# Kernel tuning notes

Hardware: AMD Instinct MI355X
Metric: run time of the kernel (lower is better)

## Reference

```python
import jax, jax.numpy as jnp
import numpy as np

# ---- static config (matches init_kwargs) ----
MO = 4            # multiplicity per output irrep: '4x0e+4x1o+4x2e'
NUM_BASIS = 10
HIDDEN = 64
N_NODES = 50000
N_EDGES = 800000

# ---------- numpy-side precompute of real Wigner-3j tensors ----------
def _sh_np(l, v):
    x, y, z = v[..., 0], v[..., 1], v[..., 2]
    if l == 0:
        return np.ones(v.shape[:-1] + (1,))
    if l == 1:
        return np.sqrt(3.0) * np.stack([x, y, z], -1)
    return np.stack([
        np.sqrt(15.0) * x * z,
        np.sqrt(15.0) * x * y,
        np.sqrt(5.0) / 2.0 * (2 * y * y - x * x - z * z),
        np.sqrt(15.0) * y * z,
        np.sqrt(15.0) / 2.0 * (z * z - x * x),
    ], -1)

def _wigner_D_np(l, R):
    # real Wigner-D consistent with _sh_np basis: sh(R v) = D @ sh(v)
    if l == 0:
        return np.ones((1, 1))
    rng = np.random.default_rng(1234 + l)
    V = rng.normal(size=(2 * l + 1, 3))
    V /= np.linalg.norm(V, axis=1, keepdims=True)
    B = _sh_np(l, V).T
    A = _sh_np(l, V @ R.T).T
    return A @ np.linalg.inv(B)

def _w3j_np(l1, l2, l3):
    rng = np.random.default_rng(42)
    rows = []
    for _ in range(3):
        Q, _ = np.linalg.qr(rng.normal(size=(3, 3)))
        if np.linalg.det(Q) < 0:
            Q = Q.copy(); Q[:, 0] *= -1.0
        K = np.kron(np.kron(_wigner_D_np(l1, Q), _wigner_D_np(l2, Q)), _wigner_D_np(l3, Q))
        rows.append(K - np.eye(K.shape[0]))
    _, _, vt = np.linalg.svd(np.concatenate(rows, 0))
    c = vt[-1]
    c = c * np.sign(c[np.argmax(np.abs(c))])
    C = c.reshape(2 * l1 + 1, 2 * l2 + 1, 2 * l3 + 1)
    return C / np.linalg.norm(C)

_SH_IRREPS = [(0, 1), (1, -1), (2, 1)]   # 1x0e + 1x1o + 1x2e
_OUT_IRREPS = [(0, 1), (1, -1), (2, 1)]  # MO x (0e, 1o, 2e)

def _build_tp(mul1, l1, p1):
    # e3nn FullyConnectedTensorProduct instructions ('uvw', component/element norm)
    ins = []
    for (l2, p2) in _SH_IRREPS:
        for io, (lo, po) in enumerate(_OUT_IRREPS):
            if abs(l1 - l2) <= lo <= l1 + l2 and p1 * p2 == po:
                ins.append({'l2': l2, 'lo': lo, 'io': io})
    fan = {}
    for j in ins:
        fan[j['io']] = fan.get(j['io'], 0) + mul1  # mul1 * mul2(=1)
    for j in ins:
        j['pw'] = float(np.sqrt((2 * j['lo'] + 1) / fan[j['io']]))
        j['C'] = _w3j_np(l1, j['l2'], j['lo'])
    return ins

INS_S = _build_tp(1, 0, 1)
INS_P = _build_tp(3, 1, -1)
INS_D = _build_tp(5, 2, 1)
WNUM_S = len(INS_S) * 1 * MO   # 12
WNUM_P = len(INS_P) * 3 * MO   # 48
WNUM_D = len(INS_D) * 5 * MO   # 80

# ---------- jax forward pieces ----------
def _sh_jnp(u):
    # component-normalized real spherical harmonics, lmax=2, e3nn convention
    x, y, z = u[:, 0], u[:, 1], u[:, 2]
    s3, s15, s5 = np.sqrt(3.0), np.sqrt(15.0), np.sqrt(5.0)
    return jnp.stack([
        jnp.ones_like(x),
        s3 * x, s3 * y, s3 * z,
        s15 * x * z, s15 * x * y,
        s5 / 2.0 * (2 * y * y - x * x - z * z),
        s15 * y * z, s15 / 2.0 * (z * z - x * x),
    ], axis=1)

def _soft_one_hot(x, end, number):
    # e3nn soft_one_hot_linspace, basis='smooth_finite', cutoff=True
    values = jnp.linspace(0.0, end, number + 2)
    step = values[1] - values[0]
    values = values[1:-1]
    diff = (x[:, None] - values) / step
    def sus(t):
        return jnp.where(t > 0, jnp.exp(-1.0 / jnp.where(t > 0, t, 1.0)), 0.0)
    return (1.14136 * np.exp(2.0)) * sus(diff + 1.0) * sus(1.0 - diff)

def _fc(x, W1, W2):
    # e3nn FullyConnectedNet([n_in, hidden, n_out], relu): weight/ sqrt(fan_in),
    # relu normalized to second moment 1 (factor sqrt(2))
    h = np.sqrt(2.0) * jax.nn.relu(x @ (W1 / np.sqrt(x.shape[1])))
    return h @ (W2 / np.sqrt(W1.shape[1]))

def _apply_tp(x1, sh, weights, ins, mul1):
    # x1: (E, mul1, 2l1+1); sh: (E, 9); weights: (E, len(ins)*mul1*MO)
    E = x1.shape[0]
    outs = [jnp.zeros((E, MO, 2 * lo + 1), x1.dtype) for lo in (0, 1, 2)]
    off = 0
    for j in ins:
        W = weights[:, off:off + mul1 * MO].reshape(E, mul1, MO)
        off += mul1 * MO
        l2 = j['l2']
        shj = sh[:, l2 * l2:(l2 + 1) * (l2 + 1)]
        C = jnp.asarray(j['C'], x1.dtype)
        outs[j['lo']] = outs[j['lo']] + j['pw'] * jnp.einsum(
            'eui,ej,ijk,euw->ewk', x1, shj, C, W)
    return jnp.concatenate([o.reshape(E, -1) for o in outs], axis=1)  # (E, 36)

def _forward(f_in, pos, W1_s, W2_s, W1_p, W2_p, W1_d, W2_d, row, col, max_radius, num_nodes):
    edge_vec = pos[row] - pos[col]                      # (E, 3)
    r = jnp.sqrt(jnp.sum(edge_vec * edge_vec, axis=1) + 1e-12)
    u = edge_vec / r[:, None]
    sh = _sh_jnp(u)                                     # (E, 9)
    emb = _soft_one_hot(r, float(max_radius), NUM_BASIS) * (NUM_BASIS ** 0.5)
    ws = _fc(emb, W1_s, W2_s)
    wp = _fc(emb, W1_p, W2_p)
    wd = _fc(emb, W1_d, W2_d)
    fm = f_in.reshape(num_nodes, 9, 9, 2)
    # tp(x0) + tp(x1) with identical weights == tp(x0 + x1) by linearity in input1
    x_s = (fm[:, 0:1, 0:1, 0] + fm[:, 0:1, 0:1, 1]).reshape(num_nodes, 1, 1)[row]
    x_p = (fm[:, 1:4, 1:4, 0] + fm[:, 1:4, 1:4, 1]).reshape(num_nodes, 3, 3)[row]
    x_d = (fm[:, 4:9, 4:9, 0] + fm[:, 4:9, 4:9, 1]).reshape(num_nodes, 5, 5)[row]
    out_s = _apply_tp(x_s, sh, ws, INS_S, 1)
    out_p = _apply_tp(x_p, sh, wp, INS_P, 3)
    out_d = _apply_tp(x_d, sh, wd, INS_D, 5)
    summand = jnp.concatenate([out_s, out_p, out_d], axis=1)   # (E, 108)
    f_out = jax.ops.segment_sum(summand, col, num_segments=num_nodes)
    num_neighbors = row.shape[0] / num_nodes
    return f_out / (num_neighbors ** 0.5)

def setup_inputs() -> dict:
    key = jax.random.key(0)
    ks = jax.random.split(key, 9)
    return {
        'f_in': jax.random.normal(ks[0], (N_NODES, 162), jnp.float32),
        'edge_index': jax.random.randint(ks[1], (2, N_EDGES), 0, N_NODES, dtype=jnp.int32),
        'pos': jax.random.normal(ks[2], (N_NODES, 3), jnp.float32),
        'max_radius': 5,
        'num_nodes': N_NODES,
        'W1_s': jax.random.normal(ks[3], (NUM_BASIS, HIDDEN), jnp.float32),
        'W2_s': jax.random.normal(ks[4], (HIDDEN, WNUM_S), jnp.float32),
        'W1_p': jax.random.normal(ks[5], (NUM_BASIS, HIDDEN), jnp.float32),
        'W2_p': jax.random.normal(ks[6], (HIDDEN, WNUM_P), jnp.float32),
        'W1_d': jax.random.normal(ks[7], (NUM_BASIS, HIDDEN), jnp.float32),
        'W2_d': jax.random.normal(ks[8], (HIDDEN, WNUM_D), jnp.float32),
    }

def reference(f_in, edge_index, pos, max_radius, num_nodes, W1_s, W2_s, W1_p, W2_p, W1_d, W2_d):
    return _forward(f_in, pos, W1_s, W2_s, W1_p, W2_p, W1_d, W2_d,
                    edge_index[0], edge_index[1], max_radius, num_nodes)
```

## Files before the change

### kernel.cpp

```cpp
#include <hip/hip_runtime.h>
#include <math.h>

#define TPB 256

#define R10   0.31622776601683794f
#define R30   0.18257418583505536f
#define R30x2 0.36514837167011072f
#define CCA (0.23904572186687872f)
#define CCB (0.20701966780270623f)
#define CCC (0.11952286093343936f)

#define TROW 144
#define RSTR 56

typedef float f4 __attribute__((ext_vector_type(4)));

__device__ __forceinline__ void atomAddF(float* p, float v) {
    __hip_atomic_fetch_add(p, v, __ATOMIC_RELAXED, __HIP_MEMORY_SCOPE_AGENT);
}

__global__ __launch_bounds__(256) void build_rec_count(const float* __restrict__ f_in,
                                                       const float* __restrict__ pos,
                                                       const int* __restrict__ eidx,
                                                       float* __restrict__ rec,
                                                       int* __restrict__ cnt,
                                                       int N, int E) {
    int i = blockIdx.x * 256 + threadIdx.x;
    if (i < N) {
        const float* f = f_in + (size_t)i * 162;
        float* r = rec + (size_t)i * RSTR;
        r[0] = pos[i * 3 + 0]; r[1] = pos[i * 3 + 1]; r[2] = pos[i * 3 + 2];
        float2 v0 = *(const float2*)f;
        r[3] = v0.x + v0.y;
#pragma unroll
        for (int u = 0; u < 3; ++u)
#pragma unroll
            for (int v = 0; v < 3; ++v) {
                float2 a = *(const float2*)(f + ((1 + u) * 9 + (1 + v)) * 2);
                r[4 + u * 3 + v] = a.x + a.y;
            }
#pragma unroll
        for (int u = 0; u < 5; ++u)
#pragma unroll
            for (int v = 0; v < 5; ++v) {
                float2 a = *(const float2*)(f + ((4 + u) * 9 + (4 + v)) * 2);
                r[16 + u * 8 + v] = a.x + a.y;
            }
    }
    if (i < E) atomicAdd(&cnt[eidx[E + i]], 1);
}

__global__ __launch_bounds__(256) void build_table(const float* __restrict__ W1s,
                                                   const float* __restrict__ W2s,
                                                   const float* __restrict__ W1p,
                                                   const float* __restrict__ W2p,
                                                   const float* __restrict__ W1d,
                                                   const float* __restrict__ W2d,
                                                   float* __restrict__ table,
                                                   float Delta, float base) {
    __shared__ float t3[192];
    const int tid = threadIdx.x;
    const float r = (float)blockIdx.x * Delta;

    const float F = (float)(1.14136 * 7.38905609893065 * 3.1622776601683795);
    float qq = r * 2.2f;
    int a0 = (int)floorf(qq) - 1;
    int ac = min(max(a0, 0), 8);
    float d0 = qq - (float)(ac + 1);
    float d0s = d0 * d0;
    float ea = (d0s < 1.f) ? F * expf(-2.f / (1.f - d0s)) : 0.f;
    float d1 = d0 - 1.f;
    float d1s = d1 * d1;
    float eb = (d1s < 1.f) ? F * expf(-2.f / (1.f - d1s)) : 0.f;

    if (tid < 192) {
        int path = tid >> 6, j = tid & 63;
        const float* W1 = (path == 0) ? W1s : (path == 1) ? W1p : W1d;
        float u = W1[ac * 64 + j];
        float v = W1[(ac + 1) * 64 + j];
        t3[tid] = fmaxf(fmaf(eb, v, ea * u), 0.f);
    }
    __syncthreads();
    if (tid >= 140) return;

    const float* W2; const float* t; int M, m; float kf; int newcol;
    if (tid < 12) {
        W2 = W2s; t = t3; M = 12; m = tid; kf = 1.f;
        int kind = m >> 2, w = m & 3;
        newcol = w * 4 + kind;
    } else if (tid < 60) {
        W2 = W2p; t = t3 + 64; M = 48; m = tid - 12;
        kf = (m < 12) ? 0.40824829046386307f
           : (m < 24) ? 0.33333333333333333f
           : (m < 36) ? 1.29099444873580560f
                      : 0.70710678118654752f;
        int kind = m / 12, u = (m % 12) >> 2, w = m & 3;
        newcol = 16 + w * 12 + u * 4 + kind;
    } else {
        W2 = W2d; t = t3 + 128; M = 80; m = tid - 60;
        kf = (m < 20) ? 0.31622776601683794f
           : (m < 40) ? 0.77459666924148340f
           : (m < 60) ? 0.2f
                      : 0.70710678118654752f;
        int kind = m / 20, u = (m % 20) >> 2, w = m & 3;
        newcol = 64 + w * 20 + u * 4 + kind;
    }
    float acc = 0.f;
#pragma unroll 4
    for (int j = 0; j < 64; ++j)
        acc = fmaf(t[j], W2[j * M + m], acc);
    table[(size_t)blockIdx.x * TROW + newcol] = acc * (base * kf);
}

__global__ __launch_bounds__(1024) void scan_kernel(int* data, int N) {
    __shared__ int wsum[16];
    const int tid = threadIdx.x;
    const int lane = tid & 63;
    const int wv = tid >> 6;
    int carry = 0;
    for (int base = 0; base < N; base += 4096) {
        int i0 = base + tid * 4;
        int v0 = (i0 + 0 < N) ? data[i0 + 0] : 0;
        int v1 = (i0 + 1 < N) ? data[i0 + 1] : 0;
        int v2 = (i0 + 2 < N) ? data[i0 + 2] : 0;
        int v3 = (i0 + 3 < N) ? data[i0 + 3] : 0;
        int s = v0 + v1 + v2 + v3;
        int sc = s;
        for (int d = 1; d < 64; d <<= 1) {
            int t = __shfl_up(sc, d);
            if (lane >= d) sc += t;
        }
        if (lane == 63) wsum[wv] = sc;
        __syncthreads();
        int woff = carry, tot = carry;
#pragma unroll
        for (int w = 0; w < 16; ++w) {
            int x = wsum[w];
            if (w < wv) woff += x;
            tot += x;
        }
        int excl = woff + (sc - s);
        if (i0 + 0 < N) data[i0 + 0] = excl;
        excl += v0;
        if (i0 + 1 < N) data[i0 + 1] = excl;
        excl += v1;
        if (i0 + 2 < N) data[i0 + 2] = excl;
        excl += v2;
        if (i0 + 3 < N) data[i0 + 3] = excl;
        carry = tot;
        __syncthreads();
    }
}

__global__ __launch_bounds__(256) void permute_rows(const int* __restrict__ eidx,
                                                    int* __restrict__ cursor,
                                                    int* __restrict__ rows, int E) {
    int e = blockIdx.x * 256 + threadIdx.x;
    if (e < E) {
        int c = eidx[E + e];
        int p = atomicAdd(&cursor[c], 1);
        rows[p] = eidx[e];
    }
}

__global__ __launch_bounds__(256) void gather_kernel(
    const float* __restrict__ rec,
    const int* __restrict__ rows,
    const int* __restrict__ cursor,
    const float* __restrict__ table,
    float* __restrict__ out,
    int N, int NB, float invDelta)
{
    const int bRole = (4 * N + 255) >> 8;
    int bid = blockIdx.x;
    int role = (bid < bRole) ? 2 : (bid < 2 * bRole) ? 1 : 0;
    int lbid = bid - ((role == 2) ? 0 : (role == 1) ? bRole : 2 * bRole);
    int idx = lbid * 256 + threadIdx.x;
    if (idx >= 4 * N) return;
    const int node = idx >> 2;
    const int w = idx & 3;

    const float* rq = rec + (size_t)node * RSTR;
    const float qx = rq[0], qy = rq[1], qz = rq[2];
    const int e0 = (node == 0) ? 0 : cursor[node - 1];
    const int e1 = cursor[node];

    float a0 = 0.f, a1 = 0.f, a2 = 0.f, a3 = 0.f, a4 = 0.f,
          a5 = 0.f, a6 = 0.f, a7 = 0.f, a8 = 0.f;

    for (int p = e0; p < e1; ++p) {
        int row = rows[p];
        const float* rr = rec + (size_t)row * RSTR;
        f4 h0 = *(const f4*)rr;
        float ex = h0[0] - qx, ey = h0[1] - qy, ez = h0[2] - qz;
        float r = sqrtf(ex * ex + ey * ey + ez * ez + 1e-12f);
        float rinv = 1.0f / r;
        float x = ex * rinv, y = ey * rinv, z = ez * rinv;

        float sh1 = 1.7320508075688772f * x;
        float sh2 = 1.7320508075688772f * y;
        float sh3 = 1.7320508075688772f * z;
        float sh4 = 3.8729833462074170f * x * z;
        float sh5 = 3.8729833462074170f * x * y;
        float sh6 = 1.1180339887498949f * (2.f * y * y - x * x - z * z);
        float sh7 = 3.8729833462074170f * y * z;
        float sh8 = 1.9364916731037085f * (z * z - x * x);

        float rn = r * invDelta;
        int bin = (int)floorf(rn);
        float f = rn - (float)bin;
        if (bin >= NB) { bin = NB - 1; f = 1.f; }
        const float* T0 = table + (size_t)bin * TROW;
        const float* T1 = T0 + TROW;

        if (role == 0) {
            f4 ta = *(const f4*)(T0 + w * 4);
            f4 tc = *(const f4*)(T1 + w * 4);
            float ws0 = fmaf(f, tc[0] - ta[0], ta[0]);
            float ws1 = fmaf(f, tc[1] - ta[1], ta[1]);
            float ws2 = fmaf(f, tc[2] - ta[2], ta[2]);
            float X = h0[3];
            a0 = fmaf(X, ws0, a0);
            float t1 = X * ws1;
            a1 = fmaf(t1, sh1, a1);
            a2 = fmaf(t1, sh2, a2);
            a3 = fmaf(t1, sh3, a3);
            float t2 = X * ws2;
            a4 = fmaf(t2, sh4, a4);
            a5 = fmaf(t2, sh5, a5);
            a6 = fmaf(t2, sh6, a6);
            a7 = fmaf(t2, sh7, a7);
            a8 = fmaf(t2, sh8, a8);
        } else if (role == 1) {
            f4 xv0 = *(const f4*)(rr + 4);
            f4 xv1 = *(const f4*)(rr + 8);
            float xp8 = rr[12];
            const float* tp0 = T0 + 16 + w * 12;
            const float* tp1 = T1 + 16 + w * 12;
#pragma unroll
            for (int u = 0; u < 3; ++u) {
                float x0 = (u == 0) ? xv0[0] : (u == 1) ? xv0[3] : xv1[2];
                float x1 = (u == 0) ? xv0[1] : (u == 1) ? xv1[0] : xv1[3];
                float x2 = (u == 0) ? xv0[2] : (u == 1) ? xv1[1] : xp8;
                f4 ta = *(const f4*)(tp0 + u * 4);
                f4 tc = *(const f4*)(tp1 + u * 4);
                f4 wv;
                wv[0] = fmaf(f, tc[0] - ta[0], ta[0]);
                wv[1] = fmaf(f, tc[1] - ta[1], ta[1]);
                wv[2] = fmaf(f, tc[2] - ta[2], ta[2]);
                wv[3] = fmaf(f, tc[3] - ta[3], ta[3]);
                float dot = x0 * sh1 + x1 * sh2 + x2 * sh3;
                float ya0 = R10 * (x0 * sh3 + x2 * sh1);
                float ya1 = R10 * (x0 * sh2 + x1 * sh1);
                float ya2 = R30 * (2.f * x1 * sh2 - x0 * sh1 - x2 * sh3);
                float ya3 = R10 * (x1 * sh3 + x2 * sh2);
                float ya4 = R10 * (x2 * sh3 - x0 * sh1);
                float yb0 = R10 * (x2 * sh4 + x1 * sh5 - x0 * sh8) - R30 * x0 * sh6;
                float yb1 = R10 * (x0 * sh5 + x2 * sh7) + R30x2 * x1 * sh6;
                float yb2 = R10 * (x0 * sh4 + x1 * sh7 + x2 * sh8) - R30 * x2 * sh6;
                a0 = fmaf(dot, wv[1], a0);
                a1 = fmaf(x0, wv[0], fmaf(yb0, wv[3], a1));
                a2 = fmaf(x1, wv[0], fmaf(yb1, wv[3], a2));
                a3 = fmaf(x2, wv[0], fmaf(yb2, wv[3], a3));
                a4 = fmaf(ya0, wv[2], a4);
                a5 = fmaf(ya1, wv[2], a5);
                a6 = fmaf(ya2, wv[2], a6);
                a7 = fmaf(ya3, wv[2], a7);
                a8 = fmaf(ya4, wv[2], a8);
            }
        } else {
            const float* td0 = T0 + 64 + w * 20;
            const float* td1 = T1 + 64 + w * 20;
#pragma unroll
            for (int u = 0; u < 5; ++u) {
                f4 xv = *(const f4*)(rr + 16 + u * 8);
                float x4 = rr[16 + u * 8 + 4];
                float x0 = xv[0], x1 = xv[1], x2 = xv[2], x3 = xv[3];
                f4 ta = *(const f4*)(td0 + u * 4);
                f4 tc = *(const f4*)(td1 + u * 4);
                f4 wv;
                wv[0] = fmaf(f, tc[0] - ta[0], ta[0]);
                wv[1] = fmaf(f, tc[1] - ta[1], ta[1]);
                wv[2] = fmaf(f, tc[2] - ta[2], ta[2]);
                wv[3] = fmaf(f, tc[3] - ta[3], ta[3]);
                float dot = x0 * sh4 + x1 * sh5 + x2 * sh6 + x3 * sh7 + x4 * sh8;
                float yb0 = R10 * (x0 * sh3 + x1 * sh2 - x4 * sh1) - R30 * x2 * sh1;
                float yb1 = R10 * (x1 * sh1 + x3 * sh3) + R30x2 * x2 * sh2;
                float yb2 = R10 * (x0 * sh1 + x3 * sh2 + x4 * sh3) - R30 * x2 * sh3;
                float yc0 = CCA * (x2 * sh4 + x0 * sh6) - CCB * (x1 * sh7 + x3 * sh5);
                float yc1 = CCB * (x1 * sh8 + x4 * sh5 - x0 * sh7 - x3 * sh4)
                          - CCC * (x1 * sh6 + x2 * sh5);
                float yc2 = CCA * (x0 * sh4 - x2 * sh6 + x4 * sh8)
                          - CCC * (x1 * sh5 + x3 * sh7);
                float yc3 = -CCB * (x0 * sh5 + x1 * sh4 + x3 * sh8 + x4 * sh7)
                          - CCC * (x2 * sh7 + x3 * sh6);
                float yc4 = CCB * (x1 * sh5 - x3 * sh7) + CCA * (x2 * sh8 + x4 * sh6);
                a0 = fmaf(dot, wv[2], a0);
                a1 = fmaf(yb0, wv[1], a1);
                a2 = fmaf(yb1, wv[1], a2);
                a3 = fmaf(yb2, wv[1], a3);
                a4 = fmaf(x0, wv[0], fmaf(yc0, wv[3], a4));
                a5 = fmaf(x1, wv[0], fmaf(yc1, wv[3], a5));
                a6 = fmaf(x2, wv[0], fmaf(yc2, wv[3], a6));
                a7 = fmaf(x3, wv[0], fmaf(yc3, wv[3], a7));
                a8 = fmaf(x4, wv[0], fmaf(yc4, wv[3], a8));
            }
        }
    }

    const int obase = (role == 0) ? 0 : (role == 1) ? 36 : 72;
    float* o = out + (size_t)node * 108 + obase;
    o[w] = a0;
    o[4 + w * 3 + 0] = a1;
    o[4 + w * 3 + 1] = a2;
    o[4 + w * 3 + 2] = a3;
    o[16 + w * 5 + 0] = a4;
    o[16 + w * 5 + 1] = a5;
    o[16 + w * 5 + 2] = a6;
    o[16 + w * 5 + 3] = a7;
    o[16 + w * 5 + 4] = a8;
}

template<int M>
__device__ __forceinline__ void fc_eval(const float* sW1T, const float* sW2,
                                        const float emb[12], float* acc)
{
#pragma unroll
    for (int m = 0; m < M; ++m) acc[m] = 0.f;
#pragma unroll 2
    for (int j = 0; j < 64; ++j) {
        const float4* w1r = (const float4*)(sW1T + j * 12);
        float4 A = w1r[0], B = w1r[1], C = w1r[2];
        float t = A.x*emb[0] + A.y*emb[1] + A.z*emb[2] + A.w*emb[3]
                + B.x*emb[4] + B.y*emb[5] + B.z*emb[6] + B.w*emb[7]
                + C.x*emb[8] + C.y*emb[9];
        t = fmaxf(t, 0.f);
        const float4* w2r = (const float4*)(sW2 + j * M);
#pragma unroll
        for (int q = 0; q < M / 4; ++q) {
            float4 V = w2r[q];
            acc[4*q+0] = fmaf(t, V.x, acc[4*q+0]);
            acc[4*q+1] = fmaf(t, V.y, acc[4*q+1]);
            acc[4*q+2] = fmaf(t, V.z, acc[4*q+2]);
            acc[4*q+3] = fmaf(t, V.w, acc[4*q+3]);
        }
    }
}

__global__ __launch_bounds__(TPB) void eqconv_edge_kernel_atomic(
    const float* __restrict__ f_in,
    const int*   __restrict__ eidx,
    const float* __restrict__ pos,
    const float* __restrict__ W1s_g, const float* __restrict__ W2s_g,
    const float* __restrict__ W1p_g, const float* __restrict__ W2p_g,
    const float* __restrict__ W1d_g, const float* __restrict__ W2d_g,
    float* __restrict__ out,
    int E, float snorm)
{
    __shared__ __align__(16) float smem[11264];
    float* tW1s = smem;
    float* tW1p = smem + 768;
    float* tW1d = smem + 1536;
    float* sW2s = smem + 2304;
    float* sW2p = smem + 3072;
    float* sW2d = smem + 6144;

    const int tid = threadIdx.x;
    const float base = 0.05590169943749474f * snorm;

    for (int idx = tid; idx < 768; idx += TPB) {
        int j = idx / 12, i = idx - j * 12;
        tW1s[idx] = (i < 10) ? W1s_g[i * 64 + j] : 0.f;
        tW1p[idx] = (i < 10) ? W1p_g[i * 64 + j] : 0.f;
        tW1d[idx] = (i < 10) ? W1d_g[i * 64 + j] : 0.f;
    }
    for (int idx = tid; idx < 768; idx += TPB)
        sW2s[idx] = W2s_g[idx] * base;
    for (int idx = tid; idx < 3072; idx += TPB) {
        int m = idx % 48;
        float k = (m < 12) ? 0.40824829046386307f
                : (m < 24) ? 0.33333333333333333f
                : (m < 36) ? 1.29099444873580560f
                           : 0.70710678118654752f;
        sW2p[idx] = W2p_g[idx] * (base * k);
    }
    for (int idx = tid; idx < 5120; idx += TPB) {
        int m = idx % 80;
        float k = (m < 20) ? 0.31622776601683794f
                : (m < 40) ? 0.77459666924148340f
                : (m < 60) ? 0.2f
                           : 0.70710678118654752f;
        sW2d[idx] = W2d_g[idx] * (base * k);
    }
    __syncthreads();

    int e = blockIdx.x * TPB + tid;
    if (e >= E) return;

    const int row = eidx[e];
    const int col = eidx[E + e];

    float ex = pos[row * 3 + 0] - pos[col * 3 + 0];
    float ey = pos[row * 3 + 1] - pos[col * 3 + 1];
    float ez = pos[row * 3 + 2] - pos[col * 3 + 2];
    float r = sqrtf(ex * ex + ey * ey + ez * ez + 1e-12f);
    float rinv = 1.0f / r;
    float x = ex * rinv, y = ey * rinv, z = ez * rinv;

    float sh1 = 1.7320508075688772f * x;
    float sh2 = 1.7320508075688772f * y;
    float sh3 = 1.7320508075688772f * z;
    float sh4 = 3.8729833462074170f * x * z;
    float sh5 = 3.8729833462074170f * x * y;
    float sh6 = 1.1180339887498949f * (2.f * y * y - x * x - z * z);
    float sh7 = 3.8729833462074170f * y * z;
    float sh8 = 1.9364916731037085f * (z * z - x * x);

    float emb[12];
    {
        const float F = (float)(1.14136 * 7.38905609893065 * 3.1622776601683795);
        const float inv_step = 2.2f;
#pragma unroll
        for (int i = 0; i < 10; ++i) {
            float v = (float)(i + 1) * (5.0f / 11.0f);
            float d = (r - v) * inv_step;
            float d2 = d * d;
            emb[i] = (d2 < 1.0f) ? F * expf(-2.0f / (1.0f - d2)) : 0.f;
        }
        emb[10] = 0.f; emb[11] = 0.f;
    }

    const float* fr = f_in + (size_t)row * 162;
    float* o = out + (size_t)col * 108;

    {
        float ws[12];
        fc_eval<12>(tW1s, sW2s, emb, ws);
        float2 v0 = *(const float2*)(fr);
        float X = v0.x + v0.y;
#pragma unroll
        for (int w = 0; w < 4; ++w) {
            atomAddF(o + w, X * ws[w]);
            float t1 = X * ws[4 + w];
            atomAddF(o + 4 + w * 3 + 0, t1 * sh1);
            atomAddF(o + 4 + w * 3 + 1, t1 * sh2);
            atomAddF(o + 4 + w * 3 + 2, t1 * sh3);
            float t2 = X * ws[8 + w];
            atomAddF(o + 16 + w * 5 + 0, t2 * sh4);
            atomAddF(o + 16 + w * 5 + 1, t2 * sh5);
            atomAddF(o + 16 + w * 5 + 2, t2 * sh6);
            atomAddF(o + 16 + w * 5 + 3, t2 * sh7);
            atomAddF(o + 16 + w * 5 + 4, t2 * sh8);
        }
    }
    {
        float wp[48];
        fc_eval<48>(tW1p, sW2p, emb, wp);
        float op0[4] = {0.f,0.f,0.f,0.f};
        float op1[12], op2[20];
#pragma unroll
        for (int t = 0; t < 12; ++t) op1[t] = 0.f;
#pragma unroll
        for (int t = 0; t < 20; ++t) op2[t] = 0.f;
#pragma unroll
        for (int u = 0; u < 3; ++u) {
            float2 a0 = *(const float2*)(fr + ((1 + u) * 9 + 1) * 2);
            float2 a1 = *(const float2*)(fr + ((1 + u) * 9 + 2) * 2);
            float2 a2 = *(const float2*)(fr + ((1 + u) * 9 + 3) * 2);
            float x0 = a0.x + a0.y, x1 = a1.x + a1.y, x2 = a2.x + a2.y;
            float dot = x0 * sh1 + x1 * sh2 + x2 * sh3;
            float ya0 = R10 * (x0 * sh3 + x2 * sh1);
            float ya1 = R10 * (x0 * sh2 + x1 * sh1);
            float ya2 = R30 * (2.f * x1 * sh2 - x0 * sh1 - x2 * sh3);
            float ya3 = R10 * (x1 * sh3 + x2 * sh2);
            float ya4 = R10 * (x2 * sh3 - x0 * sh1);
            float yb0 = R10 * (x2 * sh4 + x1 * sh5 - x0 * sh8) - R30 * x0 * sh6;
            float yb1 = R10 * (x0 * sh5 + x2 * sh7) + R30x2 * x1 * sh6;
            float yb2 = R10 * (x0 * sh4 + x1 * sh7 + x2 * sh8) - R30 * x2 * sh6;
#pragma unroll
            for (int w = 0; w < 4; ++w) {
                float wa = wp[u * 4 + w];
                float wb = wp[12 + u * 4 + w];
                float wc = wp[24 + u * 4 + w];
                float wd2 = wp[36 + u * 4 + w];
                op0[w] = fmaf(dot, wb, op0[w]);
                op1[w * 3 + 0] = fmaf(x0, wa, fmaf(yb0, wd2, op1[w * 3 + 0]));
                op1[w * 3 + 1] = fmaf(x1, wa, fmaf(yb1, wd2, op1[w * 3 + 1]));
                op1[w * 3 + 2] = fmaf(x2, wa, fmaf(yb2, wd2, op1[w * 3 + 2]));
                op2[w * 5 + 0] = fmaf(ya0, wc, op2[w * 5 + 0]);
                op2[w * 5 + 1] = fmaf(ya1, wc, op2[w * 5 + 1]);
                op2[w * 5 + 2] = fmaf(ya2, wc, op2[w * 5 + 2]);
                op2[w * 5 + 3] = fmaf(ya3, wc, op2[w * 5 + 3]);
                op2[w * 5 + 4] = fmaf(ya4, wc, op2[w * 5 + 4]);
            }
        }
#pragma unroll
        for (int w = 0; w < 4; ++w) atomAddF(o + 36 + w, op0[w]);
#pragma unroll
        for (int t = 0; t < 12; ++t) atomAddF(o + 40 + t, op1[t]);
#pragma unroll
        for (int t = 0; t < 20; ++t) atomAddF(o + 52 + t, op2[t]);
    }
    {
        float wd[80];
        fc_eval<80>(tW1d, sW2d, emb, wd);
        float od0[4] = {0.f,0.f,0.f,0.f};
        float od1[12], od2[20];
#pragma unroll
        for (int t = 0; t < 12; ++t) od1[t] = 0.f;
#pragma unroll
        for (int t = 0; t < 20; ++t) od2[t] = 0.f;
#pragma unroll
        for (int u = 0; u < 5; ++u) {
            float2 b0 = *(const float2*)(fr + ((4 + u) * 9 + 4) * 2);
            float2 b1 = *(const float2*)(fr + ((4 + u) * 9 + 5) * 2);
            float2 b2 = *(const float2*)(fr + ((4 + u) * 9 + 6) * 2);
            float2 b3 = *(const float2*)(fr + ((4 + u) * 9 + 7) * 2);
            float2 b4 = *(const float2*)(fr + ((4 + u) * 9 + 8) * 2);
            float x0 = b0.x + b0.y, x1 = b1.x + b1.y, x2 = b2.x + b2.y;
            float x3 = b3.x + b3.y, x4 = b4.x + b4.y;
            float dot = x0 * sh4 + x1 * sh5 + x2 * sh6 + x3 * sh7 + x4 * sh8;
            float yb0 = R10 * (x0 * sh3 + x1 * sh2 - x4 * sh1) - R30 * x2 * sh1;
            float yb1 = R10 * (x1 * sh1 + x3 * sh3) + R30x2 * x2 * sh2;
            float yb2 = R10 * (x0 * sh1 + x3 * sh2 + x4 * sh3) - R30 * x2 * sh3;
            float yc0 = CCA * (x2 * sh4 + x0 * sh6) - CCB * (x1 * sh7 + x3 * sh5);
            float yc1 = CCB * (x1 * sh8 + x4 * sh5 - x0 * sh7 - x3 * sh4)
                      - CCC * (x1 * sh6 + x2 * sh5);
            float yc2 = CCA * (x0 * sh4 - x2 * sh6 + x4 * sh8)
                      - CCC * (x1 * sh5 + x3 * sh7);
            float yc3 = -CCB * (x0 * sh5 + x1 * sh4 + x3 * sh8 + x4 * sh7)
                      - CCC * (x2 * sh7 + x3 * sh6);
            float yc4 = CCB * (x1 * sh5 - x3 * sh7) + CCA * (x2 * sh8 + x4 * sh6);
#pragma unroll
            for (int w = 0; w < 4; ++w) {
                float wa = wd[u * 4 + w];
                float wb = wd[20 + u * 4 + w];
                float wc = wd[40 + u * 4 + w];
                float we = wd[60 + u * 4 + w];
                od0[w] = fmaf(dot, wc, od0[w]);
                od1[w * 3 + 0] = fmaf(yb0, wb, od1[w * 3 + 0]);
                od1[w * 3 + 1] = fmaf(yb1, wb, od1[w * 3 + 1]);
                od1[w * 3 + 2] = fmaf(yb2, wb, od1[w * 3 + 2]);
                od2[w * 5 + 0] = fmaf(x0, wa, fmaf(yc0, we, od2[w * 5 + 0]));
                od2[w * 5 + 1] = fmaf(x1, wa, fmaf(yc1, we, od2[w * 5 + 1]));
                od2[w * 5 + 2] = fmaf(x2, wa, fmaf(yc2, we, od2[w * 5 + 2]));
                od2[w * 5 + 3] = fmaf(x3, wa, fmaf(yc3, we, od2[w * 5 + 3]));
                od2[w * 5 + 4] = fmaf(x4, wa, fmaf(yc4, we, od2[w * 5 + 4]));
            }
        }
#pragma unroll
        for (int w = 0; w < 4; ++w) atomAddF(o + 72 + w, od0[w]);
#pragma unroll
        for (int t = 0; t < 12; ++t) atomAddF(o + 76 + t, od1[t]);
#pragma unroll
        for (int t = 0; t < 20; ++t) atomAddF(o + 88 + t, od2[t]);
    }
}

extern "C" void kernel_launch(void* const* d_in, const int* in_sizes, int n_in,
                              void* d_out, int out_size, void* d_ws, size_t ws_size,
                              hipStream_t stream) {
    const float* f_in = (const float*)d_in[0];
    const int*   eidx = (const int*)d_in[1];
    const float* pos  = (const float*)d_in[2];
    const float* W1s = (const float*)d_in[5];
    const float* W2s = (const float*)d_in[6];
    const float* W1p = (const float*)d_in[7];
    const float* W2p = (const float*)d_in[8];
    const float* W1d = (const float*)d_in[9];
    const float* W2d = (const float*)d_in[10];

    const int E = in_sizes[1] / 2;
    const int N = in_sizes[0] / 162;
    const float snorm = (float)(1.0 / sqrt((double)E / (double)N));
    const float base = 0.05590169943749474f * snorm;
    const int eBlocks = (E + 255) / 256;

    const size_t rowsBytes = (size_t)E * sizeof(int);
    const size_t curOff = rowsBytes;
    const size_t recOff = (curOff + (size_t)N * sizeof(int) + 15) & ~((size_t)15);
    const size_t tabOff = (recOff + (size_t)N * RSTR * sizeof(float) + 15) & ~((size_t)15);

    int NB = 0;
    if (ws_size > tabOff) {
        size_t rows_avail = (ws_size - tabOff) / (TROW * sizeof(float));
        if (rows_avail >= 513) NB = (int)((rows_avail - 1) < 2048 ? (rows_avail - 1) : 2048);
    }

    if (NB >= 512) {
        int*   rows   = (int*)d_ws;
        int*   cursor = (int*)((char*)d_ws + curOff);
        float* rec    = (float*)((char*)d_ws + recOff);
        float* table  = (float*)((char*)d_ws + tabOff);
        const float Delta = 5.0f / (float)NB;
        const float invDelta = (float)NB / 5.0f;

        hipMemsetAsync(cursor, 0, (size_t)N * sizeof(int), stream);
        build_rec_count<<<eBlocks, 256, 0, stream>>>(f_in, pos, eidx, rec, cursor, N, E);
        build_table<<<NB + 1, 256, 0, stream>>>(W1s, W2s, W1p, W2p, W1d, W2d,
                                                table, Delta, base);
        scan_kernel<<<1, 1024, 0, stream>>>(cursor, N);
        permute_rows<<<eBlocks, 256, 0, stream>>>(eidx, cursor, rows, E);
        const int bRole = (4 * N + 255) / 256;
        gather_kernel<<<3 * bRole, 256, 0, stream>>>(
            rec, rows, cursor, table, (float*)d_out, N, NB, invDelta);
    } else {
        hipMemsetAsync(d_out, 0, (size_t)out_size * sizeof(float), stream);
        eqconv_edge_kernel_atomic<<<eBlocks, TPB, 0, stream>>>(
            f_in, eidx, pos, W1s, W2s, W1p, W2p, W1d, W2d,
            (float*)d_out, E, snorm);
    }
}
```

Baseline: 390.0 us.

## Sort nodes by degree, fuse per-role gather passes, replace serial scan

Replaces the single-block serial prefix scan with a parallel wave-level scan that takes block offsets through an atomic, plus a degree histogram and counting sort that orders nodes by in-degree. The gather kernel now runs one thread per (node, w) that computes all three output roles in one edge loop, so each edge's geometry and spherical harmonics are computed once instead of three times. It uses 64-thread blocks over degree-sorted nodes to cut wavefront divergence from uneven edge counts. In exchange each thread holds 27 accumulators, which raises register pressure, and the CSR segments become non-contiguous in node order, which may hurt locality.

```diff
diff --git a/kernel.cpp b/kernel.cpp
--- a/kernel.cpp
+++ b/kernel.cpp
@@ -112,43 +112,49 @@
     table[(size_t)blockIdx.x * TROW + newcol] = acc * (base * kf);
 }
 
-__global__ __launch_bounds__(1024) void scan_kernel(int* data, int N) {
-    __shared__ int wsum[16];
-    const int tid = threadIdx.x;
-    const int lane = tid & 63;
-    const int wv = tid >> 6;
-    int carry = 0;
-    for (int base = 0; base < N; base += 4096) {
-        int i0 = base + tid * 4;
-        int v0 = (i0 + 0 < N) ? data[i0 + 0] : 0;
-        int v1 = (i0 + 1 < N) ? data[i0 + 1] : 0;
-        int v2 = (i0 + 2 < N) ? data[i0 + 2] : 0;
-        int v3 = (i0 + 3 < N) ? data[i0 + 3] : 0;
-        int s = v0 + v1 + v2 + v3;
-        int sc = s;
-        for (int d = 1; d < 64; d <<= 1) {
-            int t = __shfl_up(sc, d);
-            if (lane >= d) sc += t;
-        }
-        if (lane == 63) wsum[wv] = sc;
-        __syncthreads();
-        int woff = carry, tot = carry;
-#pragma unroll
-        for (int w = 0; w < 16; ++w) {
-            int x = wsum[w];
-            if (w < wv) woff += x;
-            tot += x;
-        }
-        int excl = woff + (sc - s);
-        if (i0 + 0 < N) data[i0 + 0] = excl;
-        excl += v0;
-        if (i0 + 1 < N) data[i0 + 1] = excl;
-        excl += v1;
-        if (i0 + 2 < N) data[i0 + 2] = excl;
-        excl += v2;
-        if (i0 + 3 < N) data[i0 + 3] = excl;
-        carry = tot;
-        __syncthreads();
+__global__ __launch_bounds__(256) void alloc_kernel(const int* __restrict__ cnt,
+                                                    int* __restrict__ start,
+                                                    int* __restrict__ cursor,
+                                                    int* __restrict__ misc, int N) {
+    int i = blockIdx.x * 256 + threadIdx.x;
+    int lane = threadIdx.x & 63;
+    int c = (i < N) ? cnt[i] : 0;
+    int sc = c;
+    for (int d = 1; d < 64; d <<= 1) {
+        int t = __shfl_up(sc, d);
+        if (lane >= d) sc += t;
+    }
+    int wtot = __shfl(sc, 63);
+    int base = 0;
+    if (lane == 63) base = atomicAdd(&misc[0], wtot);
+    base = __shfl(base, 63);
+    if (i < N) {
+        int s = base + (sc - c);
+        start[i] = s;
+        cursor[i] = s;
+        atomicAdd(&misc[1 + min(c, 63)], 1);
+    }
+}
+
+__global__ void dscan_kernel(int* misc) {
+    int lane = threadIdx.x;
+    int v = misc[1 + lane];
+    int sc = v;
+    for (int d = 1; d < 64; d <<= 1) {
+        int t = __shfl_up(sc, d);
+        if (lane >= d) sc += t;
+    }
+    misc[65 + lane] = sc - v;
+}
+
+__global__ __launch_bounds__(256) void order_kernel(const int* __restrict__ cnt,
+                                                    int* __restrict__ misc,
+                                                    int* __restrict__ order, int N) {
+    int i = blockIdx.x * 256 + threadIdx.x;
+    if (i < N) {
+        int d = min(cnt[i], 63);
+        int o = atomicAdd(&misc[65 + d], 1);
+        order[o] = i;
     }
 }
 
@@ -163,30 +169,32 @@
     }
 }
 
-__global__ __launch_bounds__(256) void gather_kernel(
+__global__ __launch_bounds__(64) void gather_kernel(
     const float* __restrict__ rec,
     const int* __restrict__ rows,
-    const int* __restrict__ cursor,
+    const int* __restrict__ start,
+    const int* __restrict__ endc,
+    const int* __restrict__ order,
     const float* __restrict__ table,
     float* __restrict__ out,
     int N, int NB, float invDelta)
 {
-    const int bRole = (4 * N + 255) >> 8;
-    int bid = blockIdx.x;
-    int role = (bid < bRole) ? 2 : (bid < 2 * bRole) ? 1 : 0;
-    int lbid = bid - ((role == 2) ? 0 : (role == 1) ? bRole : 2 * bRole);
-    int idx = lbid * 256 + threadIdx.x;
+    int idx = blockIdx.x * 64 + threadIdx.x;
     if (idx >= 4 * N) return;
-    const int node = idx >> 2;
+    const int node = order[idx >> 2];
     const int w = idx & 3;
 
     const float* rq = rec + (size_t)node * RSTR;
     const float qx = rq[0], qy = rq[1], qz = rq[2];
-    const int e0 = (node == 0) ? 0 : cursor[node - 1];
-    const int e1 = cursor[node];
-
-    float a0 = 0.f, a1 = 0.f, a2 = 0.f, a3 = 0.f, a4 = 0.f,
-          a5 = 0.f, a6 = 0.f, a7 = 0.f, a8 = 0.f;
+    const int e0 = start[node];
+    const int e1 = endc[node];
+
+    float s0 = 0.f, s1 = 0.f, s2 = 0.f, s3 = 0.f, s4 = 0.f,
+          s5 = 0.f, s6 = 0.f, s7 = 0.f, s8 = 0.f;
+    float p0 = 0.f, p1 = 0.f, p2 = 0.f, p3 = 0.f, p4 = 0.f,
+          p5 = 0.f, p6 = 0.f, p7 = 0.f, p8 = 0.f;
+    float d0a = 0.f, d1a = 0.f, d2a = 0.f, d3a = 0.f, d4a = 0.f,
+          d5a = 0.f, d6a = 0.f, d7a = 0.f, d8a = 0.f;
 
     for (int p = e0; p < e1; ++p) {
         int row = rows[p];
@@ -213,25 +221,26 @@
         const float* T0 = table + (size_t)bin * TROW;
         const float* T1 = T0 + TROW;
 
-        if (role == 0) {
+        {
             f4 ta = *(const f4*)(T0 + w * 4);
             f4 tc = *(const f4*)(T1 + w * 4);
             float ws0 = fmaf(f, tc[0] - ta[0], ta[0]);
             float ws1 = fmaf(f, tc[1] - ta[1], ta[1]);
             float ws2 = fmaf(f, tc[2] - ta[2], ta[2]);
             float X = h0[3];
-            a0 = fmaf(X, ws0, a0);
+            s0 = fmaf(X, ws0, s0);
             float t1 = X * ws1;
-            a1 = fmaf(t1, sh1, a1);
-            a2 = fmaf(t1, sh2, a2);
-            a3 = fmaf(t1, sh3, a3);
+            s1 = fmaf(t1, sh1, s1);
+            s2 = fmaf(t1, sh2, s2);
+            s3 = fmaf(t1, sh3, s3);
             float t2 = X * ws2;
-            a4 = fmaf(t2, sh4, a4);
-            a5 = fmaf(t2, sh5, a5);
-            a6 = fmaf(t2, sh6, a6);
-            a7 = fmaf(t2, sh7, a7);
-            a8 = fmaf(t2, sh8, a8);
-        } else if (role == 1) {
+            s4 = fmaf(t2, sh4, s4);
+            s5 = fmaf(t2, sh5, s5);
+            s6 = fmaf(t2, sh6, s6);
+            s7 = fmaf(t2, sh7, s7);
+            s8 = fmaf(t2, sh8, s8);
+        }
+        {
             f4 xv0 = *(const f4*)(rr + 4);
             f4 xv1 = *(const f4*)(rr + 8);
             float xp8 = rr[12];
@@ -258,17 +267,18 @@
                 float yb0 = R10 * (x2 * sh4 + x1 * sh5 - x0 * sh8) - R30 * x0 * sh6;
                 float yb1 = R10 * (x0 * sh5 + x2 * sh7) + R30x2 * x1 * sh6;
                 float yb2 = R10 * (x0 * sh4 + x1 * sh7 + x2 * sh8) - R30 * x2 * sh6;
-                a0 = fmaf(dot, wv[1], a0);
-                a1 = fmaf(x0, wv[0], fmaf(yb0, wv[3], a1));
-                a2 = fmaf(x1, wv[0], fmaf(yb1, wv[3], a2));
-                a3 = fmaf(x2, wv[0], fmaf(yb2, wv[3], a3));
-                a4 = fmaf(ya0, wv[2], a4);
-                a5 = fmaf(ya1, wv[2], a5);
-                a6 = fmaf(ya2, wv[2], a6);
-                a7 = fmaf(ya3, wv[2], a7);
-                a8 = fmaf(ya4, wv[2], a8);
+                p0 = fmaf(dot, wv[1], p0);
+                p1 = fmaf(x0, wv[0], fmaf(yb0, wv[3], p1));
+                p2 = fmaf(x1, wv[0], fmaf(yb1, wv[3], p2));
+                p3 = fmaf(x2, wv[0], fmaf(yb2, wv[3], p3));
+                p4 = fmaf(ya0, wv[2], p4);
+                p5 = fmaf(ya1, wv[2], p5);
+                p6 = fmaf(ya2, wv[2], p6);
+                p7 = fmaf(ya3, wv[2], p7);
+                p8 = fmaf(ya4, wv[2], p8);
             }
-        } else {
+        }
+        {
             const float* td0 = T0 + 64 + w * 20;
             const float* td1 = T1 + 64 + w * 20;
 #pragma unroll
@@ -295,30 +305,32 @@
                 float yc3 = -CCB * (x0 * sh5 + x1 * sh4 + x3 * sh8 + x4 * sh7)
                           - CCC * (x2 * sh7 + x3 * sh6);
                 float yc4 = CCB * (x1 * sh5 - x3 * sh7) + CCA * (x2 * sh8 + x4 * sh6);
-                a0 = fmaf(dot, wv[2], a0);
-                a1 = fmaf(yb0, wv[1], a1);
-                a2 = fmaf(yb1, wv[1], a2);
-                a3 = fmaf(yb2, wv[1], a3);
-                a4 = fmaf(x0, wv[0], fmaf(yc0, wv[3], a4));
-                a5 = fmaf(x1, wv[0], fmaf(yc1, wv[3], a5));
-                a6 = fmaf(x2, wv[0], fmaf(yc2, wv[3], a6));
-                a7 = fmaf(x3, wv[0], fmaf(yc3, wv[3], a7));
-                a8 = fmaf(x4, wv[0], fmaf(yc4, wv[3], a8));
+                d0a = fmaf(dot, wv[2], d0a);
+                d1a = fmaf(yb0, wv[1], d1a);
+                d2a = fmaf(yb1, wv[1], d2a);
+                d3a = fmaf(yb2, wv[1], d3a);
+                d4a = fmaf(x0, wv[0], fmaf(yc0, wv[3], d4a));
+                d5a = fmaf(x1, wv[0], fmaf(yc1, wv[3], d5a));
+                d6a = fmaf(x2, wv[0], fmaf(yc2, wv[3], d6a));
+                d7a = fmaf(x3, wv[0], fmaf(yc3, wv[3], d7a));
+                d8a = fmaf(x4, wv[0], fmaf(yc4, wv[3], d8a));
             }
         }
     }
 
-    const int obase = (role == 0) ? 0 : (role == 1) ? 36 : 72;
-    float* o = out + (size_t)node * 108 + obase;
-    o[w] = a0;
-    o[4 + w * 3 + 0] = a1;
-    o[4 + w * 3 + 1] = a2;
-    o[4 + w * 3 + 2] = a3;
-    o[16 + w * 5 + 0] = a4;
-    o[16 + w * 5 + 1] = a5;
-    o[16 + w * 5 + 2] = a6;
-    o[16 + w * 5 + 3] = a7;
-    o[16 + w * 5 + 4] = a8;
+    float* o = out + (size_t)node * 108;
+    o[w] = s0;
+    o[4 + w * 3 + 0] = s1;  o[4 + w * 3 + 1] = s2;  o[4 + w * 3 + 2] = s3;
+    o[16 + w * 5 + 0] = s4; o[16 + w * 5 + 1] = s5; o[16 + w * 5 + 2] = s6;
+    o[16 + w * 5 + 3] = s7; o[16 + w * 5 + 4] = s8;
+    o[36 + w] = p0;
+    o[40 + w * 3 + 0] = p1; o[40 + w * 3 + 1] = p2; o[40 + w * 3 + 2] = p3;
+    o[52 + w * 5 + 0] = p4; o[52 + w * 5 + 1] = p5; o[52 + w * 5 + 2] = p6;
+    o[52 + w * 5 + 3] = p7; o[52 + w * 5 + 4] = p8;
+    o[72 + w] = d0a;
+    o[76 + w * 3 + 0] = d1a; o[76 + w * 3 + 1] = d2a; o[76 + w * 3 + 2] = d3a;
+    o[88 + w * 5 + 0] = d4a; o[88 + w * 5 + 1] = d5a; o[88 + w * 5 + 2] = d6a;
+    o[88 + w * 5 + 3] = d7a; o[88 + w * 5 + 4] = d8a;
 }
 
 template<int M>
@@ -575,11 +587,15 @@
     const float snorm = (float)(1.0 / sqrt((double)E / (double)N));
     const float base = 0.05590169943749474f * snorm;
     const int eBlocks = (E + 255) / 256;
-
-    const size_t rowsBytes = (size_t)E * sizeof(int);
-    const size_t curOff = rowsBytes;
-    const size_t recOff = (curOff + (size_t)N * sizeof(int) + 15) & ~((size_t)15);
-    const size_t tabOff = (recOff + (size_t)N * RSTR * sizeof(float) + 15) & ~((size_t)15);
+    const int nBlocks = (N + 255) / 256;
+
+    const size_t cntOff  = (size_t)E * sizeof(int);
+    const size_t miscOff = cntOff + (size_t)N * sizeof(int);
+    const size_t startOff = miscOff + 144 * sizeof(int);
+    const size_t curOff  = startOff + (size_t)N * sizeof(int);
+    const size_t ordOff  = curOff + (size_t)N * sizeof(int);
+    const size_t recOff  = (ordOff + (size_t)N * sizeof(int) + 15) & ~((size_t)15);
+    const size_t tabOff  = (recOff + (size_t)N * RSTR * sizeof(float) + 15) & ~((size_t)15);
 
     int NB = 0;
     if (ws_size > tabOff) {
@@ -589,21 +605,26 @@
 
     if (NB >= 512) {
         int*   rows   = (int*)d_ws;
+        int*   cnt    = (int*)((char*)d_ws + cntOff);
+        int*   misc   = (int*)((char*)d_ws + miscOff);
+        int*   start  = (int*)((char*)d_ws + startOff);
         int*   cursor = (int*)((char*)d_ws + curOff);
+        int*   order  = (int*)((char*)d_ws + ordOff);
         float* rec    = (float*)((char*)d_ws + recOff);
         float* table  = (float*)((char*)d_ws + tabOff);
         const float Delta = 5.0f / (float)NB;
         const float invDelta = (float)NB / 5.0f;
 
-        hipMemsetAsync(cursor, 0, (size_t)N * sizeof(int), stream);
-        build_rec_count<<<eBlocks, 256, 0, stream>>>(f_in, pos, eidx, rec, cursor, N, E);
+        hipMemsetAsync(cnt, 0, ((size_t)N + 144) * sizeof(int), stream);
+        build_rec_count<<<eBlocks, 256, 0, stream>>>(f_in, pos, eidx, rec, cnt, N, E);
         build_table<<<NB + 1, 256, 0, stream>>>(W1s, W2s, W1p, W2p, W1d, W2d,
                                                 table, Delta, base);
-        scan_kernel<<<1, 1024, 0, stream>>>(cursor, N);
+        alloc_kernel<<<nBlocks, 256, 0, stream>>>(cnt, start, cursor, misc, N);
+        dscan_kernel<<<1, 64, 0, stream>>>(misc);
+        order_kernel<<<nBlocks, 256, 0, stream>>>(cnt, misc, order, N);
         permute_rows<<<eBlocks, 256, 0, stream>>>(eidx, cursor, rows, E);
-        const int bRole = (4 * N + 255) / 256;
-        gather_kernel<<<3 * bRole, 256, 0, stream>>>(
-            rec, rows, cursor, table, (float*)d_out, N, NB, invDelta);
+        gather_kernel<<<(4 * N + 63) / 64, 64, 0, stream>>>(
+            rec, rows, start, cursor, order, table, (float*)d_out, N, NB, invDelta);
     } else {
         hipMemsetAsync(d_out, 0, (size_t)out_size * sizeof(float), stream);
         eqconv_edge_kernel_atomic<<<eBlocks, TPB, 0, stream>>>(
```

New measurement: 601.3 us. 1.54x slower.
